# Kernel tuning notes

Hardware: AMD Instinct MI355X
Metric: run time of the kernel (lower is better)

Reference implementation:

```python
import jax, jax.numpy as jnp
import numpy as np

EMBED_DIM = 256
NUM_CODES = 8192
COMMIT_COST = 0.25


def setup_inputs() -> dict:
    key = jax.random.key(0)
    k1, k2 = jax.random.split(key)
    x = jax.random.normal(k1, (16, 1024, EMBED_DIM), dtype=jnp.float32)
    # torch init is uniform(-1/K, 1/K); use small-scale normal-like init via uniform
    codebook = jax.random.uniform(k2, (NUM_CODES, EMBED_DIM), dtype=jnp.float32,
                                  minval=-1.0 / NUM_CODES, maxval=1.0 / NUM_CODES)
    return {"x": x, "codebook": codebook}


def reference(x, codebook):
    # x: [B, S, D], codebook: [K, D]
    input_shape = x.shape
    flat = x.reshape(-1, EMBED_DIM)  # [N, D]
    distances = (jnp.sum(flat * flat, axis=1, keepdims=True)
                 + jnp.sum(codebook * codebook, axis=1)
                 - 2.0 * jnp.matmul(flat, codebook.T))
    encoding_indices = jnp.argmin(distances, axis=1)  # [N]
    # one-hot @ codebook is just a gather
    quantized = jnp.take(codebook, encoding_indices, axis=0).reshape(input_shape)
    # training w/ EMA: commitment loss only (codebook updated via EMA buffers, not grad)
    commitment_loss = COMMIT_COST * jnp.mean(
        (jax.lax.stop_gradient(quantized) - x) ** 2)
    # straight-through estimator
    quantized_st = x + jax.lax.stop_gradient(quantized - x)
    indices = encoding_indices.reshape(input_shape[:-1])
    return quantized_st, indices, commitment_loss
```

## Files before the change

kernel.cpp:

```cpp
#include <hip/hip_runtime.h>

#define D 256
#define KCODES 8192
#define NTOK 16384
#define QSIZE (NTOK * D)
#define NBLK 128
#define CBS 64
#define TH 2e-4f
#define CBSCALE 4096.0f
#define UNSCALE2 4.8828125e-4f
#define CCAP 4096

typedef _Float16 f16x8 __attribute__((ext_vector_type(8)));
typedef float f32x4 __attribute__((ext_vector_type(4)));
typedef __attribute__((address_space(3))) void* lds_vp;
typedef __attribute__((address_space(1))) const void* gbl_vp;

#define P1_LDS (128 * 256 * 2 + 2 * 128 * 32 * 2)
#define P2_LDS (256 * 65 * 4)

__device__ __forceinline__ ushort f32_to_bf16(float f) {
    unsigned u = __float_as_uint(f);
    return (ushort)((u + 0x7FFFu + ((u >> 16) & 1)) >> 16);
}
__device__ __forceinline__ float bf16_to_f32(ushort h) {
    return __uint_as_float((unsigned)h << 16);
}
__device__ __forceinline__ ushort f32_to_f16(float f) {
    _Float16 h = (_Float16)f;
    ushort u; __builtin_memcpy(&u, &h, 2);
    return u;
}
__device__ __forceinline__ float rdlane(float v, int lane) {
    return __uint_as_float(__builtin_amdgcn_readlane(__float_as_uint(v), lane));
}

__global__ __launch_bounds__(256) void cvtx_kernel(const float* __restrict__ x,
                                                   ushort* __restrict__ xb,
                                                   float* __restrict__ xsq) {
    int i = blockIdx.x * 256 + threadIdx.x;
    float4 v = reinterpret_cast<const float4*>(x)[i];
    ushort4 o;
    o.x = f32_to_f16(v.x); o.y = f32_to_f16(v.y);
    o.z = f32_to_f16(v.z); o.w = f32_to_f16(v.w);
    reinterpret_cast<ushort4*>(xb)[i] = o;
    float s = v.x * v.x + v.y * v.y + v.z * v.z + v.w * v.w;
#pragma unroll
    for (int off = 32; off > 0; off >>= 1) s += __shfl_down(s, off);
    if ((threadIdx.x & 63) == 0) xsq[i >> 6] = s;
}

__global__ __launch_bounds__(256) void e2_kernel(const float* __restrict__ cb,
                                                 float* __restrict__ e2) {
    int c = blockIdx.x * 4 + (threadIdx.x >> 6);
    int lane = threadIdx.x & 63;
    float4 v = reinterpret_cast<const float4*>(cb + (size_t)c * D)[lane];
    float s = v.x * v.x + v.y * v.y + v.z * v.z + v.w * v.w;
#pragma unroll
    for (int off = 32; off > 0; off >>= 1) s += __shfl_down(s, off);
    if (lane == 0) e2[c] = s;
}

__global__ __launch_bounds__(256, 2) void pass1_kernel(
    const ushort* __restrict__ xb, const float* __restrict__ cb,
    const float* __restrict__ e2, unsigned* __restrict__ screen) {
    extern __shared__ ushort sm[];
    ushort* Bsh = sm;
    ushort* Ash = sm + 128 * 256;
    const int tid = threadIdx.x;
    const int w = tid >> 6, l = tid & 63;
    const int wr = w >> 1, wc = w & 1;
    const int n0 = blockIdx.y * 128;
    const int tc0 = blockIdx.x * (NTOK / 8);

#pragma unroll
    for (int j = 0; j < 16; ++j) {
        int c = tid + j * 256;
        int row = c >> 5, slot = c & 31;
        const float4* grow = reinterpret_cast<const float4*>(cb + (size_t)(n0 + row) * D);
        float4 f0 = grow[slot * 2];
        float4 f1 = grow[slot * 2 + 1];
        uint4 q;
        q.x = (unsigned)f32_to_f16(f0.x * CBSCALE) |
              ((unsigned)f32_to_f16(f0.y * CBSCALE) << 16);
        q.y = (unsigned)f32_to_f16(f0.z * CBSCALE) |
              ((unsigned)f32_to_f16(f0.w * CBSCALE) << 16);
        q.z = (unsigned)f32_to_f16(f1.x * CBSCALE) |
              ((unsigned)f32_to_f16(f1.y * CBSCALE) << 16);
        q.w = (unsigned)f32_to_f16(f1.z * CBSCALE) |
              ((unsigned)f32_to_f16(f1.w * CBSCALE) << 16);
        int sw = slot ^ (row & 7);
        *reinterpret_cast<uint4*>(Bsh + row * 256 + sw * 8) = q;
    }

    const int arow0 = w * 32 + (l >> 2);
    const int arow1 = arow0 + 16;
    const int asg8 = (((l & 3) ^ ((l >> 3) & 3)) << 3);

#define STAGE_A(TB, KT, BUF)                                                               \
    do {                                                                                   \
        __builtin_amdgcn_global_load_lds(                                                  \
            (gbl_vp)(xb + (size_t)((TB) + arow0) * D + (KT) * 32 + asg8),                  \
            (lds_vp)(Ash + (BUF) * 4096 + w * 1024), 16, 0, 0);                            \
        __builtin_amdgcn_global_load_lds(                                                  \
            (gbl_vp)(xb + (size_t)((TB) + arow1) * D + (KT) * 32 + asg8),                  \
            (lds_vp)(Ash + (BUF) * 4096 + w * 1024 + 512), 16, 0, 0);                      \
    } while (0)

    const int qh = l >> 4, l7 = l & 7;
    const int aslot = qh ^ (((l & 15) >> 1) & 3);
    const int arow_rd = (wr * 64 + (l & 15)) * 32 + aslot * 8;
    const int brow_rd = (wc * 64 + (l & 15)) * 256;

    float e2v[4];
#pragma unroll
    for (int nt = 0; nt < 4; ++nt)
        e2v[nt] = e2[n0 + wc * 64 + nt * 16 + (l & 15)];
    const int nb64 = blockIdx.y * 2 + wc;

    STAGE_A(tc0, 0, 0);
    __syncthreads();

    for (int tt = 0; tt < 16; ++tt) {
        const int tbase = tc0 + tt * 128;
        f32x4 acc[4][4];
#pragma unroll
        for (int mt = 0; mt < 4; ++mt)
#pragma unroll
            for (int nt = 0; nt < 4; ++nt) acc[mt][nt] = (f32x4)0.f;
#pragma unroll
        for (int kt = 0; kt < 8; ++kt) {
            const int cur = kt & 1;
            if (kt < 7) STAGE_A(tbase, kt + 1, cur ^ 1);
            else if (tt < 15) STAGE_A(tbase + 128, 0, cur ^ 1);
            const ushort* abase = Ash + cur * 4096 + arow_rd;
            f16x8 a[4], b[4];
#pragma unroll
            for (int mt = 0; mt < 4; ++mt)
                a[mt] = *reinterpret_cast<const f16x8*>(abase + mt * 512);
#pragma unroll
            for (int nt = 0; nt < 4; ++nt)
                b[nt] = *reinterpret_cast<const f16x8*>(
                    Bsh + brow_rd + nt * 4096 + (((kt * 4 + qh) ^ l7) << 3));
#pragma unroll
            for (int mt = 0; mt < 4; ++mt)
#pragma unroll
                for (int nt = 0; nt < 4; ++nt)
                    acc[mt][nt] = __builtin_amdgcn_mfma_f32_16x16x32_f16(
                        a[mt], b[nt], acc[mt][nt], 0, 0, 0);
            if (kt == 7) {
#pragma unroll
                for (int mt = 0; mt < 4; ++mt) {
#pragma unroll
                    for (int r = 0; r < 4; ++r) {
                        float v1 = fmaf(-UNSCALE2, acc[mt][0][r], e2v[0]);
                        float v2 = 3.4e38f;
                        int a1 = (l & 15);
#pragma unroll
                        for (int nt = 1; nt < 4; ++nt) {
                            float f = fmaf(-UNSCALE2, acc[mt][nt][r], e2v[nt]);
                            int idx = nt * 16 + (l & 15);
                            bool lt = f < v1;
                            v2 = lt ? v1 : fminf(v2, f);
                            a1 = lt ? idx : a1;
                            v1 = lt ? f : v1;
                        }
#pragma unroll
                        for (int off = 1; off < 16; off <<= 1) {
                            float ov1 = __shfl_xor(v1, off);
                            float ov2 = __shfl_xor(v2, off);
                            int oa1 = __shfl_xor(a1, off);
                            float nv2 = fminf(fminf(v2, ov2), fmaxf(v1, ov1));
                            bool take = ov1 < v1;
                            v1 = take ? ov1 : v1;
                            a1 = take ? oa1 : a1;
                            v2 = nv2;
                        }
                        if ((l & 15) == 0) {
                            int token = tbase + wr * 64 + mt * 16 + (l >> 4) * 4 + r;
                            ushort m1b = f32_to_bf16(v1);
                            unsigned big = (v2 - bf16_to_f32(m1b) > TH) ? 1u : 0u;
                            screen[(size_t)token * NBLK + nb64] =
                                ((unsigned)m1b << 16) | ((unsigned)a1 << 1) | big;
                        }
                    }
                }
            }
            __syncthreads();
        }
    }
#undef STAGE_A
}

__global__ __launch_bounds__(256) void pass2a_kernel(
    const unsigned* __restrict__ screen, unsigned long long* __restrict__ bestKey,
    unsigned* __restrict__ cand, unsigned* __restrict__ counts,
    float* __restrict__ out) {
    const int tid = threadIdx.x;
    const int w = tid >> 6, l = tid & 63;
    const int token = blockIdx.x * 4 + w;
    if (blockIdx.x == 0 && tid == 0) out[(size_t)QSIZE + NTOK] = 0.f;

    uint2 u2 = reinterpret_cast<const uint2*>(screen + (size_t)token * NBLK)[l];
    float ma = bf16_to_f32((ushort)(u2.x >> 16));
    float mb = bf16_to_f32((ushort)(u2.y >> 16));
    float v1, v2; unsigned pk; int blk;
    if (mb < ma) { v1 = mb; v2 = ma; pk = u2.y; blk = 2 * l + 1; }
    else         { v1 = ma; v2 = mb; pk = u2.x; blk = 2 * l; }
#pragma unroll
    for (int off = 1; off < 64; off <<= 1) {
        float ov1 = __shfl_xor(v1, off);
        float ov2 = __shfl_xor(v2, off);
        unsigned opk = __shfl_xor(pk, off);
        int oblk = __shfl_xor(blk, off);
        float nv2 = fminf(fminf(v2, ov2), fmaxf(v1, ov1));
        bool take = ov1 < v1;
        v1 = take ? ov1 : v1;
        pk = take ? opk : pk;
        blk = take ? oblk : blk;
        v2 = nv2;
    }
    bool decided = ((pk & 1u) != 0u) && (v2 - v1 > TH);
    if (l == 0)
        bestKey[token] = decided
            ? (unsigned long long)(unsigned)(blk * 64 + (int)((pk >> 1) & 63u))
            : 0xFFFFFFFFFFFFFFFFULL;
    if (!decided) {
        float thr = v1 + TH;
        if (ma <= thr) {
            unsigned s = atomicAdd(&counts[2 * l], 1u);
            if (s < CCAP) cand[(size_t)(2 * l) * CCAP + s] = (unsigned)token;
        }
        if (mb <= thr) {
            unsigned s = atomicAdd(&counts[2 * l + 1], 1u);
            if (s < CCAP) cand[(size_t)(2 * l + 1) * CCAP + s] = (unsigned)token;
        }
    }
}

__global__ __launch_bounds__(256, 2) void pass2b_kernel(
    const float* __restrict__ x, const float* __restrict__ cb,
    const float* __restrict__ e2, const float* __restrict__ xsq,
    const unsigned* __restrict__ cand, const unsigned* __restrict__ counts,
    unsigned long long* __restrict__ bestKey) {
    extern __shared__ float csh[];
    const int tid = threadIdx.x;
    const int nb = blockIdx.x >> 2;
    const int quarter = blockIdx.x & 3;
    int cnt = (int)counts[nb];
    if (cnt > CCAP) cnt = CCAP;
    if (quarter * 16 >= cnt) return;

#pragma unroll
    for (int r = 0; r < 16; ++r) {
        int i = r * 256 + tid;
        int row = i >> 6, kq = i & 63;
        float4 v = reinterpret_cast<const float4*>(cb + (size_t)(nb * CBS + row) * D)[kq];
        csh[(kq * 4 + 0) * 65 + row] = v.x;
        csh[(kq * 4 + 1) * 65 + row] = v.y;
        csh[(kq * 4 + 2) * 65 + row] = v.z;
        csh[(kq * 4 + 3) * 65 + row] = v.w;
    }
    __syncthreads();

    const int w = tid >> 6, j = tid & 63;
    const float e2v = e2[nb * CBS + j];
    const int ci0 = nb * CBS + j;
    const float4* X4 = reinterpret_cast<const float4*>(x);
    const unsigned* clist = cand + (size_t)nb * CCAP;
    const int slot = quarter * 4 + w;
    const int p0 = slot * 4;
    if (p0 >= cnt) return;

    for (int p = p0; p < cnt; p += 64) {
        int i1 = p + 1 < cnt ? p + 1 : cnt - 1;
        int i2 = p + 2 < cnt ? p + 2 : cnt - 1;
        int i3 = p + 3 < cnt ? p + 3 : cnt - 1;
        int t0 = (int)clist[p],  t1 = (int)clist[i1];
        int t2 = (int)clist[i2], t3 = (int)clist[i3];
        float4 v0 = X4[(size_t)t0 * 64 + j];
        float4 v1 = X4[(size_t)t1 * 64 + j];
        float4 v2 = X4[(size_t)t2 * 64 + j];
        float4 v3 = X4[(size_t)t3 * 64 + j];
        float a0 = 0.f, a1 = 0.f, a2 = 0.f, a3 = 0.f;
#pragma unroll
        for (int kq = 0; kq < 64; ++kq) {
            float c0 = csh[(kq * 4 + 0) * 65 + j];
            float c1 = csh[(kq * 4 + 1) * 65 + j];
            float c2 = csh[(kq * 4 + 2) * 65 + j];
            float c3 = csh[(kq * 4 + 3) * 65 + j];
            a0 = fmaf(rdlane(v0.x, kq), c0, a0);
            a0 = fmaf(rdlane(v0.y, kq), c1, a0);
            a0 = fmaf(rdlane(v0.z, kq), c2, a0);
            a0 = fmaf(rdlane(v0.w, kq), c3, a0);
            a1 = fmaf(rdlane(v1.x, kq), c0, a1);
            a1 = fmaf(rdlane(v1.y, kq), c1, a1);
            a1 = fmaf(rdlane(v1.z, kq), c2, a1);
            a1 = fmaf(rdlane(v1.w, kq), c3, a1);
            a2 = fmaf(rdlane(v2.x, kq), c0, a2);
            a2 = fmaf(rdlane(v2.y, kq), c1, a2);
            a2 = fmaf(rdlane(v2.z, kq), c2, a2);
            a2 = fmaf(rdlane(v2.w, kq), c3, a2);
            a3 = fmaf(rdlane(v3.x, kq), c0, a3);
            a3 = fmaf(rdlane(v3.y, kq), c1, a3);
            a3 = fmaf(rdlane(v3.z, kq), c2, a3);
            a3 = fmaf(rdlane(v3.w, kq), c3, a3);
        }
        float av[4] = {a0, a1, a2, a3};
        int tv[4] = {t0, t1, t2, t3};
#pragma unroll
        for (int g = 0; g < 4; ++g) {
            float dd = fmaf(-2.f, av[g], xsq[tv[g]] + e2v);
            int ci = ci0;
#pragma unroll
            for (int off = 1; off < 64; off <<= 1) {
                float od = __shfl_xor(dd, off);
                int oc = __shfl_xor(ci, off);
                if (od < dd || (od == dd && oc < ci)) { dd = od; ci = oc; }
            }
            if (j == 0) {
                unsigned u = __float_as_uint(dd);
                u = (u & 0x80000000u) ? ~u : (u | 0x80000000u);
                unsigned long long key =
                    ((unsigned long long)u << 32) | (unsigned)ci;
                atomicMin(bestKey + tv[g], key);
            }
        }
    }
}

__global__ __launch_bounds__(256) void gather_kernel(
    const float* __restrict__ x, const float* __restrict__ cb,
    const unsigned long long* __restrict__ bestKey,
    float* __restrict__ out, float* __restrict__ partial) {
    __shared__ float red[4];
    const int token = blockIdx.x;
    const int tid = threadIdx.x;
    int idx = (int)(bestKey[token] & 0xFFFFFFFFULL);
    if ((unsigned)idx >= (unsigned)KCODES) idx = 0;
    float q = cb[(size_t)idx * D + tid];
    float xv = x[(size_t)token * D + tid];
    out[(size_t)token * D + tid] = q;
    float d = q - xv;
    d = d * d;
#pragma unroll
    for (int off = 32; off > 0; off >>= 1) d += __shfl_down(d, off);
    if ((tid & 63) == 0) red[tid >> 6] = d;
    __syncthreads();
    if (tid == 0) {
        partial[token] = red[0] + red[1] + red[2] + red[3];
        out[(size_t)QSIZE + token] = (float)idx;
    }
}

__global__ __launch_bounds__(256) void loss_kernel(const float* __restrict__ partial,
                                                   float* __restrict__ out) {
    __shared__ float red[4];
    int gid = blockIdx.x * 256 + threadIdx.x;
    float s = partial[gid];
#pragma unroll
    for (int off = 32; off > 0; off >>= 1) s += __shfl_down(s, off);
    if ((threadIdx.x & 63) == 0) red[threadIdx.x >> 6] = s;
    __syncthreads();
    if (threadIdx.x == 0) {
        float total = red[0] + red[1] + red[2] + red[3];
        atomicAdd(out + (size_t)QSIZE + NTOK, 0.25f * total / (float)QSIZE);
    }
}

extern "C" void kernel_launch(void* const* d_in, const int* in_sizes, int n_in,
                              void* d_out, int out_size, void* d_ws, size_t ws_size,
                              hipStream_t stream) {
    const float* x = (const float*)d_in[0];
    const float* cb = (const float*)d_in[1];
    float* out = (float*)d_out;
    float* ws = (float*)d_ws;

    ushort* xb = (ushort*)d_out;
    unsigned* screen = (unsigned*)((char*)d_out + 8388608);
    unsigned* cand = (unsigned*)d_out;

    float* e2 = ws;
    float* xsq = ws + 8192;
    unsigned* counts = (unsigned*)(ws + 8192 + 16384);
    float* partial = ws + 8192 + 2 * 16384;
    unsigned long long* bestKey = (unsigned long long*)(ws + 8192 + 3 * 16384);

    hipFuncSetAttribute((const void*)pass1_kernel,
                        hipFuncAttributeMaxDynamicSharedMemorySize, P1_LDS);
    hipFuncSetAttribute((const void*)pass2b_kernel,
                        hipFuncAttributeMaxDynamicSharedMemorySize, P2_LDS);

    cvtx_kernel<<<QSIZE / 1024, 256, 0, stream>>>(x, xb, xsq);
    e2_kernel<<<KCODES / 4, 256, 0, stream>>>(cb, e2);
    pass1_kernel<<<dim3(8, KCODES / 128), 256, P1_LDS, stream>>>(xb, cb, e2, screen);
    hipMemsetAsync(counts, 0, NBLK * sizeof(unsigned), stream);
    pass2a_kernel<<<NTOK / 4, 256, 0, stream>>>(screen, bestKey, cand, counts, out);
    pass2b_kernel<<<4 * NBLK, 256, P2_LDS, stream>>>(
        x, cb, e2, xsq, cand, counts, bestKey);
    gather_kernel<<<NTOK, 256, 0, stream>>>(x, cb, bestKey, out, partial);
    loss_kernel<<<NTOK / 256, 256, 0, stream>>>(partial, out);
}
```

Measured before the change: 360.6 us.

## Restructure pass1 to 64-code tiles with direct A loads; fuse prep kernels

Merges the x-conversion, codebook-norm and counts-clear steps into one prep kernel, which drops two launches and a memset. Pass1 now keeps only a 64-code B tile in static LDS and has each wave read its 64-token A fragments straight from global memory. This removes the LDS-staged, double-buffered A pipeline and its per-k-step barriers. Smaller LDS use lets the kernel declare 4 blocks per CU, but A reuse across waves is lost and global A traffic doubles because each block covers half as many codes.

```diff
diff --git a/kernel.cpp b/kernel.cpp
--- a/kernel.cpp
+++ b/kernel.cpp
@@ -13,10 +13,7 @@
 
 typedef _Float16 f16x8 __attribute__((ext_vector_type(8)));
 typedef float f32x4 __attribute__((ext_vector_type(4)));
-typedef __attribute__((address_space(3))) void* lds_vp;
-typedef __attribute__((address_space(1))) const void* gbl_vp;
-
-#define P1_LDS (128 * 256 * 2 + 2 * 128 * 32 * 2)
+
 #define P2_LDS (256 * 65 * 4)
 
 __device__ __forceinline__ ushort f32_to_bf16(float f) {
@@ -35,46 +32,47 @@
     return __uint_as_float(__builtin_amdgcn_readlane(__float_as_uint(v), lane));
 }
 
-__global__ __launch_bounds__(256) void cvtx_kernel(const float* __restrict__ x,
-                                                   ushort* __restrict__ xb,
-                                                   float* __restrict__ xsq) {
-    int i = blockIdx.x * 256 + threadIdx.x;
-    float4 v = reinterpret_cast<const float4*>(x)[i];
-    ushort4 o;
-    o.x = f32_to_f16(v.x); o.y = f32_to_f16(v.y);
-    o.z = f32_to_f16(v.z); o.w = f32_to_f16(v.w);
-    reinterpret_cast<ushort4*>(xb)[i] = o;
-    float s = v.x * v.x + v.y * v.y + v.z * v.z + v.w * v.w;
-#pragma unroll
-    for (int off = 32; off > 0; off >>= 1) s += __shfl_down(s, off);
-    if ((threadIdx.x & 63) == 0) xsq[i >> 6] = s;
-}
-
-__global__ __launch_bounds__(256) void e2_kernel(const float* __restrict__ cb,
-                                                 float* __restrict__ e2) {
-    int c = blockIdx.x * 4 + (threadIdx.x >> 6);
-    int lane = threadIdx.x & 63;
-    float4 v = reinterpret_cast<const float4*>(cb + (size_t)c * D)[lane];
-    float s = v.x * v.x + v.y * v.y + v.z * v.z + v.w * v.w;
-#pragma unroll
-    for (int off = 32; off > 0; off >>= 1) s += __shfl_down(s, off);
-    if (lane == 0) e2[c] = s;
-}
-
-__global__ __launch_bounds__(256, 2) void pass1_kernel(
+__global__ __launch_bounds__(256) void prep_kernel(
+    const float* __restrict__ x, ushort* __restrict__ xb,
+    float* __restrict__ xsq, const float* __restrict__ cb,
+    float* __restrict__ e2, unsigned* __restrict__ counts) {
+    const int bid = blockIdx.x;
+    const int tid = threadIdx.x;
+    if (bid == 0 && tid < NBLK) counts[tid] = 0;
+    if (bid < 4096) {
+        int i = bid * 256 + tid;
+        float4 v = reinterpret_cast<const float4*>(x)[i];
+        ushort4 o;
+        o.x = f32_to_f16(v.x); o.y = f32_to_f16(v.y);
+        o.z = f32_to_f16(v.z); o.w = f32_to_f16(v.w);
+        reinterpret_cast<ushort4*>(xb)[i] = o;
+        float s = v.x * v.x + v.y * v.y + v.z * v.z + v.w * v.w;
+#pragma unroll
+        for (int off = 32; off > 0; off >>= 1) s += __shfl_down(s, off);
+        if ((tid & 63) == 0) xsq[i >> 6] = s;
+    } else {
+        int c = (bid - 4096) * 4 + (tid >> 6);
+        int lane = tid & 63;
+        float4 v = reinterpret_cast<const float4*>(cb + (size_t)c * D)[lane];
+        float s = v.x * v.x + v.y * v.y + v.z * v.z + v.w * v.w;
+#pragma unroll
+        for (int off = 32; off > 0; off >>= 1) s += __shfl_down(s, off);
+        if (lane == 0) e2[c] = s;
+    }
+}
+
+__global__ __launch_bounds__(256, 4) void pass1_kernel(
     const ushort* __restrict__ xb, const float* __restrict__ cb,
     const float* __restrict__ e2, unsigned* __restrict__ screen) {
-    extern __shared__ ushort sm[];
-    ushort* Bsh = sm;
-    ushort* Ash = sm + 128 * 256;
+    __shared__ ushort Bsh[64 * 256];
     const int tid = threadIdx.x;
     const int w = tid >> 6, l = tid & 63;
-    const int wr = w >> 1, wc = w & 1;
-    const int n0 = blockIdx.y * 128;
-    const int tc0 = blockIdx.x * (NTOK / 8);
-
-#pragma unroll
-    for (int j = 0; j < 16; ++j) {
+    const int nb = blockIdx.y;
+    const int n0 = nb * 64;
+    const int tc0 = blockIdx.x * 2048;
+
+#pragma unroll
+    for (int j = 0; j < 8; ++j) {
         int c = tid + j * 256;
         int row = c >> 5, slot = c & 31;
         const float4* grow = reinterpret_cast<const float4*>(cb + (size_t)(n0 + row) * D);
@@ -92,37 +90,21 @@
         int sw = slot ^ (row & 7);
         *reinterpret_cast<uint4*>(Bsh + row * 256 + sw * 8) = q;
     }
-
-    const int arow0 = w * 32 + (l >> 2);
-    const int arow1 = arow0 + 16;
-    const int asg8 = (((l & 3) ^ ((l >> 3) & 3)) << 3);
-
-#define STAGE_A(TB, KT, BUF)                                                               \
-    do {                                                                                   \
-        __builtin_amdgcn_global_load_lds(                                                  \
-            (gbl_vp)(xb + (size_t)((TB) + arow0) * D + (KT) * 32 + asg8),                  \
-            (lds_vp)(Ash + (BUF) * 4096 + w * 1024), 16, 0, 0);                            \
-        __builtin_amdgcn_global_load_lds(                                                  \
-            (gbl_vp)(xb + (size_t)((TB) + arow1) * D + (KT) * 32 + asg8),                  \
-            (lds_vp)(Ash + (BUF) * 4096 + w * 1024 + 512), 16, 0, 0);                      \
-    } while (0)
-
-    const int qh = l >> 4, l7 = l & 7;
-    const int aslot = qh ^ (((l & 15) >> 1) & 3);
-    const int arow_rd = (wr * 64 + (l & 15)) * 32 + aslot * 8;
-    const int brow_rd = (wc * 64 + (l & 15)) * 256;
-
+    __syncthreads();
+
+    const int qh = l >> 4, l7 = l & 7, lm = l & 15;
+    const ushort* Bbase = Bsh + lm * 256;
     float e2v[4];
 #pragma unroll
     for (int nt = 0; nt < 4; ++nt)
-        e2v[nt] = e2[n0 + wc * 64 + nt * 16 + (l & 15)];
-    const int nb64 = blockIdx.y * 2 + wc;
-
-    STAGE_A(tc0, 0, 0);
-    __syncthreads();
-
-    for (int tt = 0; tt < 16; ++tt) {
-        const int tbase = tc0 + tt * 128;
+        e2v[nt] = e2[n0 + nt * 16 + lm];
+
+    for (int tt = 0; tt < 8; ++tt) {
+        const int tbase = tc0 + tt * 256 + w * 64;
+        const ushort* At0 = xb + (size_t)(tbase + lm) * D + qh * 8;
+        const ushort* At1 = At0 + 16 * D;
+        const ushort* At2 = At0 + 32 * D;
+        const ushort* At3 = At0 + 48 * D;
         f32x4 acc[4][4];
 #pragma unroll
         for (int mt = 0; mt < 4; ++mt)
@@ -130,66 +112,59 @@
             for (int nt = 0; nt < 4; ++nt) acc[mt][nt] = (f32x4)0.f;
 #pragma unroll
         for (int kt = 0; kt < 8; ++kt) {
-            const int cur = kt & 1;
-            if (kt < 7) STAGE_A(tbase, kt + 1, cur ^ 1);
-            else if (tt < 15) STAGE_A(tbase + 128, 0, cur ^ 1);
-            const ushort* abase = Ash + cur * 4096 + arow_rd;
             f16x8 a[4], b[4];
-#pragma unroll
-            for (int mt = 0; mt < 4; ++mt)
-                a[mt] = *reinterpret_cast<const f16x8*>(abase + mt * 512);
+            a[0] = *reinterpret_cast<const f16x8*>(At0 + kt * 32);
+            a[1] = *reinterpret_cast<const f16x8*>(At1 + kt * 32);
+            a[2] = *reinterpret_cast<const f16x8*>(At2 + kt * 32);
+            a[3] = *reinterpret_cast<const f16x8*>(At3 + kt * 32);
 #pragma unroll
             for (int nt = 0; nt < 4; ++nt)
                 b[nt] = *reinterpret_cast<const f16x8*>(
-                    Bsh + brow_rd + nt * 4096 + (((kt * 4 + qh) ^ l7) << 3));
+                    Bbase + nt * 4096 + (((kt * 4 + qh) ^ l7) << 3));
 #pragma unroll
             for (int mt = 0; mt < 4; ++mt)
 #pragma unroll
                 for (int nt = 0; nt < 4; ++nt)
                     acc[mt][nt] = __builtin_amdgcn_mfma_f32_16x16x32_f16(
                         a[mt], b[nt], acc[mt][nt], 0, 0, 0);
-            if (kt == 7) {
-#pragma unroll
-                for (int mt = 0; mt < 4; ++mt) {
-#pragma unroll
-                    for (int r = 0; r < 4; ++r) {
-                        float v1 = fmaf(-UNSCALE2, acc[mt][0][r], e2v[0]);
-                        float v2 = 3.4e38f;
-                        int a1 = (l & 15);
-#pragma unroll
-                        for (int nt = 1; nt < 4; ++nt) {
-                            float f = fmaf(-UNSCALE2, acc[mt][nt][r], e2v[nt]);
-                            int idx = nt * 16 + (l & 15);
-                            bool lt = f < v1;
-                            v2 = lt ? v1 : fminf(v2, f);
-                            a1 = lt ? idx : a1;
-                            v1 = lt ? f : v1;
-                        }
-#pragma unroll
-                        for (int off = 1; off < 16; off <<= 1) {
-                            float ov1 = __shfl_xor(v1, off);
-                            float ov2 = __shfl_xor(v2, off);
-                            int oa1 = __shfl_xor(a1, off);
-                            float nv2 = fminf(fminf(v2, ov2), fmaxf(v1, ov1));
-                            bool take = ov1 < v1;
-                            v1 = take ? ov1 : v1;
-                            a1 = take ? oa1 : a1;
-                            v2 = nv2;
-                        }
-                        if ((l & 15) == 0) {
-                            int token = tbase + wr * 64 + mt * 16 + (l >> 4) * 4 + r;
-                            ushort m1b = f32_to_bf16(v1);
-                            unsigned big = (v2 - bf16_to_f32(m1b) > TH) ? 1u : 0u;
-                            screen[(size_t)token * NBLK + nb64] =
-                                ((unsigned)m1b << 16) | ((unsigned)a1 << 1) | big;
-                        }
-                    }
+        }
+#pragma unroll
+        for (int mt = 0; mt < 4; ++mt) {
+#pragma unroll
+            for (int r = 0; r < 4; ++r) {
+                float v1 = fmaf(-UNSCALE2, acc[mt][0][r], e2v[0]);
+                float v2 = 3.4e38f;
+                int a1 = lm;
+#pragma unroll
+                for (int nt = 1; nt < 4; ++nt) {
+                    float f = fmaf(-UNSCALE2, acc[mt][nt][r], e2v[nt]);
+                    int idx = nt * 16 + lm;
+                    bool lt = f < v1;
+                    v2 = lt ? v1 : fminf(v2, f);
+                    a1 = lt ? idx : a1;
+                    v1 = lt ? f : v1;
+                }
+#pragma unroll
+                for (int off = 1; off < 16; off <<= 1) {
+                    float ov1 = __shfl_xor(v1, off);
+                    float ov2 = __shfl_xor(v2, off);
+                    int oa1 = __shfl_xor(a1, off);
+                    float nv2 = fminf(fminf(v2, ov2), fmaxf(v1, ov1));
+                    bool take = ov1 < v1;
+                    v1 = take ? ov1 : v1;
+                    a1 = take ? oa1 : a1;
+                    v2 = nv2;
+                }
+                if (lm == 0) {
+                    int token = tbase + mt * 16 + (l >> 4) * 4 + r;
+                    ushort m1b = f32_to_bf16(v1);
+                    unsigned big = (v2 - bf16_to_f32(m1b) > TH) ? 1u : 0u;
+                    screen[(size_t)token * NBLK + nb] =
+                        ((unsigned)m1b << 16) | ((unsigned)a1 << 1) | big;
                 }
             }
-            __syncthreads();
-        }
-    }
-#undef STAGE_A
+        }
+    }
 }
 
 __global__ __launch_bounds__(256) void pass2a_kernel(
@@ -386,15 +361,11 @@
     float* partial = ws + 8192 + 2 * 16384;
     unsigned long long* bestKey = (unsigned long long*)(ws + 8192 + 3 * 16384);
 
-    hipFuncSetAttribute((const void*)pass1_kernel,
-                        hipFuncAttributeMaxDynamicSharedMemorySize, P1_LDS);
     hipFuncSetAttribute((const void*)pass2b_kernel,
                         hipFuncAttributeMaxDynamicSharedMemorySize, P2_LDS);
 
-    cvtx_kernel<<<QSIZE / 1024, 256, 0, stream>>>(x, xb, xsq);
-    e2_kernel<<<KCODES / 4, 256, 0, stream>>>(cb, e2);
-    pass1_kernel<<<dim3(8, KCODES / 128), 256, P1_LDS, stream>>>(xb, cb, e2, screen);
-    hipMemsetAsync(counts, 0, NBLK * sizeof(unsigned), stream);
+    prep_kernel<<<4096 + KCODES / 4, 256, 0, stream>>>(x, xb, xsq, cb, e2, counts);
+    pass1_kernel<<<dim3(8, NBLK), 256, 0, stream>>>(xb, cb, e2, screen);
     pass2a_kernel<<<NTOK / 4, 256, 0, stream>>>(screen, bestKey, cand, counts, out);
     pass2b_kernel<<<4 * NBLK, 256, P2_LDS, stream>>>(
         x, cb, e2, xsq, cand, counts, bestKey);
```

Result: slower. 489.0 us (+35.6%).
